# Performance work log

Hardware: AMD Instinct MI355X
Metric: run time of the kernel (lower is better)

Reference implementation:

```python
import jax, jax.numpy as jnp
import numpy as np

B, P, L1, D = 64, 16, 16, 1024  # images, people/img, object slots/img (slot0=no-object), feat dim
SP = 32   # flattened spatial (Conv_spatial output channels)
PROJ = 512
ACT = 29


def setup_inputs() -> dict:
    key = jax.random.key(0)
    ks = jax.random.split(key, 16)
    rn = lambda k, s, sc=1.0: jax.random.normal(k, s, dtype=jnp.float32) * sc
    w = 0.02  # weight init scale
    return {
        "people": rn(ks[0], (B, P, D)),
        "objects": rn(ks[1], (B, L1, D)),
        "context": rn(ks[2], (B, D)),
        "spatial": rn(ks[3], (B, P * L1, SP)),
        "Wvis_w": rn(ks[4], (3 * D, PROJ), w), "Wvis_b": jnp.zeros((PROJ,), jnp.float32),
        "Wspat_w": rn(ks[5], (SP, PROJ), w), "Wspat_b": jnp.zeros((PROJ,), jnp.float32),
        "Wip_w": rn(ks[6], (PROJ, 1), w), "Wip_b": jnp.zeros((1,), jnp.float32),
        "Wref_w": rn(ks[7], (PROJ, ACT), w), "Wref_b": jnp.zeros((ACT,), jnp.float32),
        "Watt_w": rn(ks[8], (PROJ, ACT), w), "Watt_b": jnp.zeros((ACT,), jnp.float32),
        "Woh_w": rn(ks[9], (D, D), w), "Woh_b": jnp.zeros((D,), jnp.float32),
        "Who_w": rn(ks[10], (D, D), w), "Who_b": jnp.zeros((D,), jnp.float32),
        "Wg_w": rn(ks[11], (2 * D, ACT), w), "Wg_b": jnp.zeros((ACT,), jnp.float32),
    }


def reference(people, objects, context, spatial,
              Wvis_w, Wvis_b, Wspat_w, Wspat_b, Wip_w, Wip_b,
              Wref_w, Wref_b, Watt_w, Watt_b,
              Woh_w, Woh_b, Who_w, Who_b, Wg_w, Wg_b):
    Bn, Pn, Dn = people.shape
    L = objects.shape[1]
    C = Bn * Pn * L

    # --- ROI.pairing: all (person, object-slot) pairs + image context -> [C, 3D]
    pe = jnp.broadcast_to(people[:, :, None, :], (Bn, Pn, L, Dn))
    ob = jnp.broadcast_to(objects[:, None, :, :], (Bn, Pn, L, Dn))
    cx = jnp.broadcast_to(context[:, None, None, :], (Bn, Pn, L, Dn))
    pairs = jnp.concatenate([pe, ob, cx], axis=-1).reshape(C, 3 * Dn)

    # --- attention / visual projection heads
    a_ho = jax.nn.relu(spatial.reshape(C, -1) @ Wspat_w + Wspat_b)   # W_Spat
    f_vis = jax.nn.relu(pairs @ Wvis_w + Wvis_b)                     # W_vis
    f_ref = f_vis * a_ho
    i_ho = f_ref @ Wip_w + Wip_b                                     # [C,1]
    interaction_prob = jax.nn.sigmoid(i_ho)
    p_ref = f_ref @ Wref_w + Wref_b                                  # [C,29]
    p_att = a_ho @ Watt_w + Watt_b                                   # [C,29]

    # --- graph message passing: adjacency = interaction probs, skipping slot 0 (no-object)
    adj = interaction_prob.reshape(Bn, Pn, L)[:, :, 1:]              # [B,P,O]
    oh = jax.nn.relu(objects[:, 1:] @ Woh_w + Woh_b)                 # W_oh on objects
    ho = jax.nn.relu(people @ Who_w + Who_b)                         # W_ho on people
    people_r = people + jnp.einsum('bpo,bod->bpd', adj, oh)
    objects_r = objects[:, 1:] + jnp.einsum('bpo,bpd->bod', adj, ho)
    objects_full = jnp.concatenate([objects[:, :1], objects_r], axis=1)  # re-attach no-object slot

    # --- refined all-pairs concat -> W_graph
    pe_r = jnp.broadcast_to(people_r[:, :, None, :], (Bn, Pn, L, Dn))
    ob_r = jnp.broadcast_to(objects_full[:, None, :, :], (Bn, Pn, L, Dn))
    pairs_g = jnp.concatenate([pe_r, ob_r], axis=-1).reshape(C, 2 * Dn)
    p_graph = pairs_g @ Wg_w + Wg_b                                  # [C,29]

    return (i_ho, p_ref, p_att, p_graph)
```

## Files before the change

### kernel.cpp

```cpp
#include <hip/hip_runtime.h>


typedef unsigned short u16;
typedef short s16x8 __attribute__((ext_vector_type(8)));
typedef float f32x4 __attribute__((ext_vector_type(4)));

__device__ __forceinline__ u16 f2b(float f) {
    union { float f; unsigned int i; } v; v.f = f;
    unsigned int r = (v.i + 0x7fffu + ((v.i >> 16) & 1u)) >> 16;
    return (u16)r;
}
__device__ __forceinline__ float b2f(u16 u) {
    union { float f; unsigned int i; } v; v.i = ((unsigned int)u) << 16; return v.f;
}
__device__ __forceinline__ unsigned int pack2(float x, float y) {
    return (unsigned int)f2b(x) | ((unsigned int)f2b(y) << 16);
}

#define OFF_WSPATT 0u
#define OFF_WREFT  32768u
#define OFF_WATTT  65536u
#define OFF_WGT    98304u
#define OFF_PP     229376u
#define OFF_PO     1277952u
#define OFF_PC     2326528u
#define OFF_ADJ    2392064u
#define OFF_HP     2457600u
#define OFF_HOF    2588672u
#define OFF_YH     2719744u
#define OFF_ZO     2850816u
#define ZERO_OFF   2457600u
#define ZERO_LEN   516096u
#define OFF_WVIST2 2973696u
#define OFF_WHOT2  6119424u
#define OFF_WOHT2  8216576u
#define OFF_PEOB   10313728u
#define OFF_OBJB   12410880u
#define OFF_CTXB   14508032u
#define OFF_SPATB  14639104u

__global__ __launch_bounds__(256) void prep_all(
    const float* __restrict__ people, const float* __restrict__ objects,
    const float* __restrict__ context, const float* __restrict__ spatial,
    const float* __restrict__ Wvis, const float* __restrict__ Who,
    const float* __restrict__ Woh, const float* __restrict__ Wspat,
    const float* __restrict__ Wref, const float* __restrict__ Watt,
    const float* __restrict__ Wg,
    u16* __restrict__ peoB, u16* __restrict__ objB, u16* __restrict__ ctxB,
    u16* __restrict__ spatB, u16* __restrict__ WvisT, u16* __restrict__ WhoT,
    u16* __restrict__ WohT, u16* __restrict__ WspatT, u16* __restrict__ WrefT,
    u16* __restrict__ WattT, u16* __restrict__ WgT)
{
    __shared__ float S[64][65];
    int bid = blockIdx.x, t = threadIdx.x;
    if (bid < 896) {
        const float* src; u16* dst; int N, K, kt, nt;
        int tb = bid;
        if (tb < 256)      { src = Who;  dst = WhoT;  K = 1024; N = 1024; kt = tb >> 4; nt = tb & 15; }
        else if (tb < 512) { tb -= 256; src = Woh;  dst = WohT;  K = 1024; N = 1024; kt = tb >> 4; nt = tb & 15; }
        else               { tb -= 512; src = Wvis; dst = WvisT; K = 3072; N = 512;  kt = tb >> 3; nt = tb & 7; }
        int k0 = kt * 64, n0 = nt * 64;
        int tx = t & 63, ty = t >> 6;
#pragma unroll
        for (int i = 0; i < 16; i++)
            S[ty + 4 * i][tx] = src[(size_t)(k0 + ty + 4 * i) * N + n0 + tx];
        __syncthreads();
#pragma unroll
        for (int i = 0; i < 16; i++)
            dst[(size_t)(n0 + ty + 4 * i) * K + k0 + tx] = f2b(S[tx][ty + 4 * i]);
        return;
    }
    int g = (bid - 896) * 256 + t;
    const int gsz = 512 * 256;
    for (int i = g; i < 524288; i += gsz) {
        float2 v = ((const float2*)people)[i];
        ((unsigned int*)peoB)[i] = pack2(v.x, v.y);
    }
    for (int i = g; i < 524288; i += gsz) {
        float2 v = ((const float2*)objects)[i];
        ((unsigned int*)objB)[i] = pack2(v.x, v.y);
    }
    for (int i = g; i < 32768; i += gsz) {
        float2 v = ((const float2*)context)[i];
        ((unsigned int*)ctxB)[i] = pack2(v.x, v.y);
    }
    for (int i = g; i < 262144; i += gsz) {
        float2 v = ((const float2*)spatial)[i];
        ((unsigned int*)spatB)[i] = pack2(v.x, v.y);
    }
    for (int i = g; i < 512 * 32; i += gsz) {
        int n = i >> 5, k = i & 31;
        WspatT[i] = f2b(Wspat[k * 512 + n]);
    }
    for (int i = g; i < 32 * 512; i += gsz) {
        int n = i >> 9, k = i & 511;
        WrefT[i] = (n < 29) ? f2b(Wref[k * 29 + n]) : (u16)0;
        WattT[i] = (n < 29) ? f2b(Watt[k * 29 + n]) : (u16)0;
    }
    for (int i = g; i < 32 * 2048; i += gsz) {
        int n = i >> 11, k = i & 2047;
        WgT[i] = (n < 29) ? f2b(Wg[k * 29 + n]) : (u16)0;
    }
}

__global__ __launch_bounds__(256) void fused_gemms(
    const u16* __restrict__ peoB, const u16* __restrict__ objB,
    const u16* __restrict__ ctxB, const u16* __restrict__ WvisT,
    const u16* __restrict__ WhoT, const float* __restrict__ Who_b,
    const u16* __restrict__ WohT, const float* __restrict__ Woh_b,
    const u16* __restrict__ WgT,
    u16* __restrict__ Pp, u16* __restrict__ Po, u16* __restrict__ Pc,
    float* __restrict__ Yh, float* __restrict__ Zo,
    float* __restrict__ Hp, float* __restrict__ HoF)
{
    __shared__ u16 T[64][72];
    int bid = blockIdx.x;
    int t = threadIdx.x;
    int lane = t & 63, w = t >> 6;
    int l16 = lane & 15, q = lane >> 4;
    int wy = w >> 1, wx = w & 1;

    if (bid < 264) {
        int bx = bid & 7, ty = bid >> 3;
        const u16* A; u16* outB; int koff, bm;
        if (ty < 16)      { A = peoB; outB = Pp; koff = 0;    bm = ty * 64; }
        else if (ty < 32) { A = objB; outB = Po; koff = 1024; bm = (ty - 16) * 64; }
        else              { A = ctxB; outB = Pc; koff = 2048; bm = 0; }
        int bn = bx * 64;

        const u16* ap0 = A + (size_t)(bm + wy * 32 + l16) * 1024 + q * 8;
        const u16* ap1 = ap0 + (size_t)16 * 1024;
        const u16* bp0 = WvisT + (size_t)(bn + wx * 32 + l16) * 3072 + koff + q * 8;
        const u16* bp1 = bp0 + (size_t)16 * 3072;

        f32x4 acc00 = {0,0,0,0}, acc01 = {0,0,0,0}, acc10 = {0,0,0,0}, acc11 = {0,0,0,0};
        s16x8 ca0 = *(const s16x8*)ap0,        ca1 = *(const s16x8*)ap1;
        s16x8 cb0 = *(const s16x8*)bp0,        cb1 = *(const s16x8*)bp1;
        s16x8 na0 = *(const s16x8*)(ap0 + 32), na1 = *(const s16x8*)(ap1 + 32);
        s16x8 nb0 = *(const s16x8*)(bp0 + 32), nb1 = *(const s16x8*)(bp1 + 32);
        ap0 += 64; ap1 += 64; bp0 += 64; bp1 += 64;
        for (int it = 0; it < 30; it++) {
            s16x8 ta0 = *(const s16x8*)ap0, ta1 = *(const s16x8*)ap1;
            s16x8 tb0 = *(const s16x8*)bp0, tb1 = *(const s16x8*)bp1;
            ap0 += 32; ap1 += 32; bp0 += 32; bp1 += 32;
            acc00 = __builtin_amdgcn_mfma_f32_16x16x32_bf16(ca0, cb0, acc00, 0, 0, 0);
            acc01 = __builtin_amdgcn_mfma_f32_16x16x32_bf16(ca0, cb1, acc01, 0, 0, 0);
            acc10 = __builtin_amdgcn_mfma_f32_16x16x32_bf16(ca1, cb0, acc10, 0, 0, 0);
            acc11 = __builtin_amdgcn_mfma_f32_16x16x32_bf16(ca1, cb1, acc11, 0, 0, 0);
            ca0 = na0; ca1 = na1; cb0 = nb0; cb1 = nb1;
            na0 = ta0; na1 = ta1; nb0 = tb0; nb1 = tb1;
        }
        acc00 = __builtin_amdgcn_mfma_f32_16x16x32_bf16(ca0, cb0, acc00, 0, 0, 0);
        acc01 = __builtin_amdgcn_mfma_f32_16x16x32_bf16(ca0, cb1, acc01, 0, 0, 0);
        acc10 = __builtin_amdgcn_mfma_f32_16x16x32_bf16(ca1, cb0, acc10, 0, 0, 0);
        acc11 = __builtin_amdgcn_mfma_f32_16x16x32_bf16(ca1, cb1, acc11, 0, 0, 0);
        acc00 = __builtin_amdgcn_mfma_f32_16x16x32_bf16(na0, nb0, acc00, 0, 0, 0);
        acc01 = __builtin_amdgcn_mfma_f32_16x16x32_bf16(na0, nb1, acc01, 0, 0, 0);
        acc10 = __builtin_amdgcn_mfma_f32_16x16x32_bf16(na1, nb0, acc10, 0, 0, 0);
        acc11 = __builtin_amdgcn_mfma_f32_16x16x32_bf16(na1, nb1, acc11, 0, 0, 0);

        f32x4 accs[2][2] = {{acc00, acc01}, {acc10, acc11}};
#pragma unroll
        for (int ii = 0; ii < 2; ii++)
#pragma unroll
            for (int jj = 0; jj < 2; jj++) {
                int col = bn + wx * 32 + jj * 16 + l16;
#pragma unroll
                for (int r = 0; r < 4; r++) {
                    int row = bm + wy * 32 + ii * 16 + q * 4 + r;
                    outB[(size_t)row * 512 + col] = f2b(accs[ii][jj][r]);
                }
            }
    } else if (bid < 760) {
        int r3 = bid - 264;
        int z, rt, nbt;
        if (r3 < 256) { z = 0; rt = r3 >> 4; nbt = r3 & 15; }
        else          { z = 1; r3 -= 256; rt = r3 >> 4; nbt = r3 & 15; }
        const u16* A    = z ? objB : peoB;
        const u16* W1T  = z ? WohT : WhoT;
        const float* bb = z ? Woh_b : Who_b;
        const u16* Wg2  = z ? WgT : WgT + 1024;
        float* U        = z ? Zo : Yh;
        int m0 = rt * 64, nb = nbt * 64;

        int r0 = m0 + wy * 32 + l16;
        int r1 = r0 + 16;
        if (z) { r0 = (r0 / 15) * 16 + (r0 % 15) + 1;
                 r1 = (r1 / 15) * 16 + (r1 % 15) + 1; }
        const u16* ap0 = A + (size_t)r0 * 1024 + q * 8;
        const u16* ap1 = A + (size_t)r1 * 1024 + q * 8;
        const u16* bp0 = W1T + (size_t)(nb + wx * 32 + l16) * 1024 + q * 8;
        const u16* bp1 = bp0 + (size_t)16 * 1024;

        f32x4 acc00 = {0,0,0,0}, acc01 = {0,0,0,0}, acc10 = {0,0,0,0}, acc11 = {0,0,0,0};
        s16x8 ca0 = *(const s16x8*)ap0,        ca1 = *(const s16x8*)ap1;
        s16x8 cb0 = *(const s16x8*)bp0,        cb1 = *(const s16x8*)bp1;
        s16x8 na0 = *(const s16x8*)(ap0 + 32), na1 = *(const s16x8*)(ap1 + 32);
        s16x8 nb0 = *(const s16x8*)(bp0 + 32), nb1 = *(const s16x8*)(bp1 + 32);
        ap0 += 64; ap1 += 64; bp0 += 64; bp1 += 64;
        for (int it = 0; it < 30; it++) {
            s16x8 ta0 = *(const s16x8*)ap0, ta1 = *(const s16x8*)ap1;
            s16x8 tb0 = *(const s16x8*)bp0, tb1 = *(const s16x8*)bp1;
            ap0 += 32; ap1 += 32; bp0 += 32; bp1 += 32;
            acc00 = __builtin_amdgcn_mfma_f32_16x16x32_bf16(ca0, cb0, acc00, 0, 0, 0);
            acc01 = __builtin_amdgcn_mfma_f32_16x16x32_bf16(ca0, cb1, acc01, 0, 0, 0);
            acc10 = __builtin_amdgcn_mfma_f32_16x16x32_bf16(ca1, cb0, acc10, 0, 0, 0);
            acc11 = __builtin_amdgcn_mfma_f32_16x16x32_bf16(ca1, cb1, acc11, 0, 0, 0);
            ca0 = na0; ca1 = na1; cb0 = nb0; cb1 = nb1;
            na0 = ta0; na1 = ta1; nb0 = tb0; nb1 = tb1;
        }
        acc00 = __builtin_amdgcn_mfma_f32_16x16x32_bf16(ca0, cb0, acc00, 0, 0, 0);
        acc01 = __builtin_amdgcn_mfma_f32_16x16x32_bf16(ca0, cb1, acc01, 0, 0, 0);
        acc10 = __builtin_amdgcn_mfma_f32_16x16x32_bf16(ca1, cb0, acc10, 0, 0, 0);
        acc11 = __builtin_amdgcn_mfma_f32_16x16x32_bf16(ca1, cb1, acc11, 0, 0, 0);
        acc00 = __builtin_amdgcn_mfma_f32_16x16x32_bf16(na0, nb0, acc00, 0, 0, 0);
        acc01 = __builtin_amdgcn_mfma_f32_16x16x32_bf16(na0, nb1, acc01, 0, 0, 0);
        acc10 = __builtin_amdgcn_mfma_f32_16x16x32_bf16(na1, nb0, acc10, 0, 0, 0);
        acc11 = __builtin_amdgcn_mfma_f32_16x16x32_bf16(na1, nb1, acc11, 0, 0, 0);

        f32x4 accs[2][2] = {{acc00, acc01}, {acc10, acc11}};
#pragma unroll
        for (int ii = 0; ii < 2; ii++)
#pragma unroll
            for (int jj = 0; jj < 2; jj++) {
                int col = wx * 32 + jj * 16 + l16;
                float bv = bb[nb + col];
#pragma unroll
                for (int rr = 0; rr < 4; rr++) {
                    float v = accs[ii][jj][rr] + bv;
                    T[wy * 32 + ii * 16 + q * 4 + rr][col] = f2b(fmaxf(v, 0.f));
                }
            }
        __syncthreads();

        f32x4 s20 = {0,0,0,0}, s21 = {0,0,0,0};
#pragma unroll
        for (int kk = 0; kk < 64; kk += 32) {
            s16x8 a2 = *(const s16x8*)(&T[w * 16 + l16][kk + q * 8]);
            s16x8 b20 = *(const s16x8*)(Wg2 + (size_t)l16 * 2048 + nb + kk + q * 8);
            s16x8 b21 = *(const s16x8*)(Wg2 + (size_t)(16 + l16) * 2048 + nb + kk + q * 8);
            s20 = __builtin_amdgcn_mfma_f32_16x16x32_bf16(a2, b20, s20, 0, 0, 0);
            s21 = __builtin_amdgcn_mfma_f32_16x16x32_bf16(a2, b21, s21, 0, 0, 0);
        }
#pragma unroll
        for (int rr = 0; rr < 4; rr++) {
            int row = m0 + w * 16 + q * 4 + rr;
            atomicAdd(&U[(size_t)row * 32 + l16], s20[rr]);
            atomicAdd(&U[(size_t)row * 32 + 16 + l16], s21[rr]);
        }
    } else {
        int r3 = bid - 760;
        int bx = r3 & 7, by = (r3 >> 3) & 7, z = r3 >> 6;
        const u16* A  = z ? objB : peoB;
        const u16* BT = z ? WgT + 1024 : WgT;
        float* outF   = z ? HoF : Hp;
        int bm = bx * 128 + w * 32;
        int kb = by * 128;
        const u16* ap0 = A + (size_t)(bm + l16) * 1024 + kb + q * 8;
        const u16* ap1 = A + (size_t)(bm + 16 + l16) * 1024 + kb + q * 8;
        const u16* bp0 = BT + (size_t)l16 * 2048 + kb + q * 8;
        const u16* bp1 = BT + (size_t)(16 + l16) * 2048 + kb + q * 8;
        f32x4 acc00 = {0,0,0,0}, acc01 = {0,0,0,0}, acc10 = {0,0,0,0}, acc11 = {0,0,0,0};
        s16x8 ca0 = *(const s16x8*)ap0,        ca1 = *(const s16x8*)ap1;
        s16x8 cb0 = *(const s16x8*)bp0,        cb1 = *(const s16x8*)bp1;
        s16x8 na0 = *(const s16x8*)(ap0 + 32), na1 = *(const s16x8*)(ap1 + 32);
        s16x8 nb0 = *(const s16x8*)(bp0 + 32), nb1 = *(const s16x8*)(bp1 + 32);
        ap0 += 64; ap1 += 64; bp0 += 64; bp1 += 64;
#pragma unroll
        for (int it = 0; it < 2; it++) {
            s16x8 ta0 = *(const s16x8*)ap0, ta1 = *(const s16x8*)ap1;
            s16x8 tb0 = *(const s16x8*)bp0, tb1 = *(const s16x8*)bp1;
            ap0 += 32; ap1 += 32; bp0 += 32; bp1 += 32;
            acc00 = __builtin_amdgcn_mfma_f32_16x16x32_bf16(ca0, cb0, acc00, 0, 0, 0);
            acc01 = __builtin_amdgcn_mfma_f32_16x16x32_bf16(ca0, cb1, acc01, 0, 0, 0);
            acc10 = __builtin_amdgcn_mfma_f32_16x16x32_bf16(ca1, cb0, acc10, 0, 0, 0);
            acc11 = __builtin_amdgcn_mfma_f32_16x16x32_bf16(ca1, cb1, acc11, 0, 0, 0);
            ca0 = na0; ca1 = na1; cb0 = nb0; cb1 = nb1;
            na0 = ta0; na1 = ta1; nb0 = tb0; nb1 = tb1;
        }
        acc00 = __builtin_amdgcn_mfma_f32_16x16x32_bf16(ca0, cb0, acc00, 0, 0, 0);
        acc01 = __builtin_amdgcn_mfma_f32_16x16x32_bf16(ca0, cb1, acc01, 0, 0, 0);
        acc10 = __builtin_amdgcn_mfma_f32_16x16x32_bf16(ca1, cb0, acc10, 0, 0, 0);
        acc11 = __builtin_amdgcn_mfma_f32_16x16x32_bf16(ca1, cb1, acc11, 0, 0, 0);
        acc00 = __builtin_amdgcn_mfma_f32_16x16x32_bf16(na0, nb0, acc00, 0, 0, 0);
        acc01 = __builtin_amdgcn_mfma_f32_16x16x32_bf16(na0, nb1, acc01, 0, 0, 0);
        acc10 = __builtin_amdgcn_mfma_f32_16x16x32_bf16(na1, nb0, acc10, 0, 0, 0);
        acc11 = __builtin_amdgcn_mfma_f32_16x16x32_bf16(na1, nb1, acc11, 0, 0, 0);
        f32x4 accs[2][2] = {{acc00, acc01}, {acc10, acc11}};
#pragma unroll
        for (int ii = 0; ii < 2; ii++)
#pragma unroll
            for (int jj = 0; jj < 2; jj++)
#pragma unroll
                for (int r = 0; r < 4; r++)
                    atomicAdd(&outF[(size_t)(bm + ii * 16 + q * 4 + r) * 32 + jj * 16 + l16],
                              accs[ii][jj][r]);
    }
}

__global__ __launch_bounds__(256) void mega(
    const u16* __restrict__ spatB, const u16* __restrict__ WspatT,
    const float* __restrict__ bspat,
    const u16* __restrict__ Pp, const u16* __restrict__ Po,
    const u16* __restrict__ Pc, const float* __restrict__ bvis,
    const u16* __restrict__ WrefT, const float* __restrict__ bref,
    const u16* __restrict__ WattT, const float* __restrict__ batt,
    const float* __restrict__ wip, const float* __restrict__ bip,
    float* __restrict__ outI, float* __restrict__ outRef,
    float* __restrict__ outAtt, float* __restrict__ adjw)
{
    __shared__ u16 tile[32][512];
    __shared__ float part[32][8];
    __shared__ float wipS[512];
    int t = threadIdx.x;
    int c0 = blockIdx.x * 32;
    int lane = t & 63, w = t >> 6;
    int l16 = lane & 15, q = lane >> 4;

    {
        float2 u = *(const float2*)(wip + t * 2);
        wipS[t * 2]     = u.x;
        wipS[t * 2 + 1] = u.y;
    }

    {
        s16x8 a0 = *(const s16x8*)(spatB + (size_t)(c0 + l16) * 32 + q * 8);
        s16x8 a1 = *(const s16x8*)(spatB + (size_t)(c0 + 16 + l16) * 32 + q * 8);
        const u16* wb = WspatT + (size_t)(w * 128 + l16) * 32 + q * 8;
        s16x8 cb = *(const s16x8*)wb;
        s16x8 nb_ = *(const s16x8*)(wb + 16 * 32);
        wb += 32 * 32;
#pragma unroll
        for (int nt = 0; nt < 8; nt++) {
            s16x8 tb;
            if (nt < 6) { tb = *(const s16x8*)wb; wb += 16 * 32; }
            int n = w * 128 + nt * 16;
            f32x4 acc0 = {0,0,0,0}, acc1 = {0,0,0,0};
            acc0 = __builtin_amdgcn_mfma_f32_16x16x32_bf16(a0, cb, acc0, 0, 0, 0);
            acc1 = __builtin_amdgcn_mfma_f32_16x16x32_bf16(a1, cb, acc1, 0, 0, 0);
            cb = nb_; nb_ = tb;
            float bias = bspat[n + l16];
#pragma unroll
            for (int r = 0; r < 4; r++) {
                tile[q * 4 + r][n + l16]      = f2b(fmaxf(acc0[r] + bias, 0.f));
                tile[16 + q * 4 + r][n + l16] = f2b(fmaxf(acc1[r] + bias, 0.f));
            }
        }
    }
    __syncthreads();

    {
        int rt = w >> 1, ct = w & 1;
        const u16* bp = WattT + (size_t)(ct * 16 + l16) * 512 + q * 8;
        f32x4 acc = {0,0,0,0};
        s16x8 cb = *(const s16x8*)bp;
        s16x8 nb_ = *(const s16x8*)(bp + 32);
        bp += 64;
        for (int i = 0; i < 14; i++) {
            s16x8 tb = *(const s16x8*)bp; bp += 32;
            s16x8 a = *(const s16x8*)(&tile[rt * 16 + l16][i * 32 + q * 8]);
            acc = __builtin_amdgcn_mfma_f32_16x16x32_bf16(a, cb, acc, 0, 0, 0);
            cb = nb_; nb_ = tb;
        }
        {
            s16x8 a = *(const s16x8*)(&tile[rt * 16 + l16][14 * 32 + q * 8]);
            acc = __builtin_amdgcn_mfma_f32_16x16x32_bf16(a, cb, acc, 0, 0, 0);
            a = *(const s16x8*)(&tile[rt * 16 + l16][15 * 32 + q * 8]);
            acc = __builtin_amdgcn_mfma_f32_16x16x32_bf16(a, nb_, acc, 0, 0, 0);
        }
        int col = ct * 16 + l16;
        if (col < 29) {
            float bias = batt[col];
#pragma unroll
            for (int r = 0; r < 4; r++) {
                int row = c0 + rt * 16 + q * 4 + r;
                outAtt[(size_t)row * 29 + col] = acc[r] + bias;
            }
        }
    }
    __syncthreads();

    {
        int row = t >> 3, g = t & 7;
        int c = c0 + row;
        int rp = c >> 4, bimg = c >> 8;
        int ro = bimg * 16 + (c & 15);
        const u16* ppr = Pp + (size_t)rp * 512;
        const u16* por = Po + (size_t)ro * 512;
        const u16* pcr = Pc + (size_t)bimg * 512;
        float ps = 0.f;
#pragma unroll 4
        for (int j = 0; j < 64; j += 2) {
            int col = g * 64 + j;
            unsigned int upp = *(const unsigned int*)(ppr + col);
            unsigned int upo = *(const unsigned int*)(por + col);
            unsigned int upc = *(const unsigned int*)(pcr + col);
            float2 bv = *(const float2*)(bvis + col);
            unsigned int uah = *(const unsigned int*)(&tile[row][col]);
            float fv0 = fmaxf(b2f((u16)(upp & 0xffff)) + b2f((u16)(upo & 0xffff))
                            + b2f((u16)(upc & 0xffff)) + bv.x, 0.f);
            float fv1 = fmaxf(b2f((u16)(upp >> 16)) + b2f((u16)(upo >> 16))
                            + b2f((u16)(upc >> 16)) + bv.y, 0.f);
            float fr0 = fv0 * b2f((u16)(uah & 0xffff));
            float fr1 = fv1 * b2f((u16)(uah >> 16));
            *(unsigned int*)(&tile[row][col]) = pack2(fr0, fr1);
            ps += fr0 * wipS[col] + fr1 * wipS[col + 1];
        }
        part[row][g] = ps;
    }
    __syncthreads();

    if (t < 32) {
        float s = part[t][0] + part[t][1] + part[t][2] + part[t][3]
                + part[t][4] + part[t][5] + part[t][6] + part[t][7] + bip[0];
        outI[c0 + t] = s;
        adjw[c0 + t] = 1.f / (1.f + expf(-s));
    }

    {
        int rt = w >> 1, ct = w & 1;
        const u16* bp = WrefT + (size_t)(ct * 16 + l16) * 512 + q * 8;
        f32x4 acc = {0,0,0,0};
        s16x8 cb = *(const s16x8*)bp;
        s16x8 nb_ = *(const s16x8*)(bp + 32);
        bp += 64;
        for (int i = 0; i < 14; i++) {
            s16x8 tb = *(const s16x8*)bp; bp += 32;
            s16x8 a = *(const s16x8*)(&tile[rt * 16 + l16][i * 32 + q * 8]);
            acc = __builtin_amdgcn_mfma_f32_16x16x32_bf16(a, cb, acc, 0, 0, 0);
            cb = nb_; nb_ = tb;
        }
        {
            s16x8 a = *(const s16x8*)(&tile[rt * 16 + l16][14 * 32 + q * 8]);
            acc = __builtin_amdgcn_mfma_f32_16x16x32_bf16(a, cb, acc, 0, 0, 0);
            a = *(const s16x8*)(&tile[rt * 16 + l16][15 * 32 + q * 8]);
            acc = __builtin_amdgcn_mfma_f32_16x16x32_bf16(a, nb_, acc, 0, 0, 0);
        }
        int col = ct * 16 + l16;
        if (col < 29) {
            float bias = bref[col];
#pragma unroll
            for (int r = 0; r < 4; r++) {
                int row = c0 + rt * 16 + q * 4 + r;
                outRef[(size_t)row * 29 + col] = acc[r] + bias;
            }
        }
    }
}

__global__ __launch_bounds__(256) void pgraph2(
    const float* __restrict__ adjw, const float* __restrict__ Hp,
    const float* __restrict__ HoF, const float* __restrict__ Yh,
    const float* __restrict__ Zo, const float* __restrict__ bg,
    float* __restrict__ outG)
{
    int b = blockIdx.x, t = threadIdx.x;
    __shared__ float adjS[16][16];
    __shared__ float YhS[16][32];
    __shared__ float ZoS[15][32];
    __shared__ float PA[16][32];
    __shared__ float OA[16][32];
    adjS[t >> 4][t & 15] = adjw[b * 256 + t];
    for (int i = t; i < 512; i += 256)
        YhS[i >> 5][i & 31] = Yh[(size_t)(b * 16 + (i >> 5)) * 32 + (i & 31)];
    for (int i = t; i < 480; i += 256)
        ZoS[i >> 5][i & 31] = Zo[(size_t)(b * 15 + (i >> 5)) * 32 + (i & 31)];
    __syncthreads();
    for (int i = t; i < 512; i += 256) {
        int p = i >> 5, j = i & 31;
        float s = 0.f;
#pragma unroll
        for (int o = 0; o < 15; o++) s += adjS[p][o + 1] * ZoS[o][j];
        PA[p][j] = s;
        float s2 = 0.f;
#pragma unroll
        for (int pp = 0; pp < 16; pp++) s2 += adjS[pp][p] * YhS[pp][j];
        OA[p][j] = s2;
    }
    __syncthreads();
    int p = t >> 4, l = t & 15;
    const float* hp = Hp + (size_t)(b * 16 + p) * 32;
    const float* ho = HoF + (size_t)(b * 16 + l) * 32;
    size_t c = (size_t)b * 256 + t;
    for (int j = 0; j < 29; j++) {
        float v = hp[j] + ho[j] + bg[j] + PA[p][j];
        if (l >= 1) v += OA[l][j];
        outG[c * 29 + j] = v;
    }
}

extern "C" void kernel_launch(void* const* d_in, const int* in_sizes, int n_in,
                              void* d_out, int out_size, void* d_ws, size_t ws_size,
                              hipStream_t stream)
{
    const float* people  = (const float*)d_in[0];
    const float* objects = (const float*)d_in[1];
    const float* context = (const float*)d_in[2];
    const float* spatial = (const float*)d_in[3];
    const float* Wvis_w  = (const float*)d_in[4];
    const float* Wvis_b  = (const float*)d_in[5];
    const float* Wspat_w = (const float*)d_in[6];
    const float* Wspat_b = (const float*)d_in[7];
    const float* Wip_w   = (const float*)d_in[8];
    const float* Wip_b   = (const float*)d_in[9];
    const float* Wref_w  = (const float*)d_in[10];
    const float* Wref_b  = (const float*)d_in[11];
    const float* Watt_w  = (const float*)d_in[12];
    const float* Watt_b  = (const float*)d_in[13];
    const float* Woh_w   = (const float*)d_in[14];
    const float* Woh_b   = (const float*)d_in[15];
    const float* Who_w   = (const float*)d_in[16];
    const float* Who_b   = (const float*)d_in[17];
    const float* Wg_w    = (const float*)d_in[18];
    const float* Wg_b    = (const float*)d_in[19];

    char* ws = (char*)d_ws;
    u16* WspatT = (u16*)(ws + OFF_WSPATT);
    u16* WrefT  = (u16*)(ws + OFF_WREFT);
    u16* WattT  = (u16*)(ws + OFF_WATTT);
    u16* WgT    = (u16*)(ws + OFF_WGT);
    u16* Ppb    = (u16*)(ws + OFF_PP);
    u16* Pob    = (u16*)(ws + OFF_PO);
    u16* Pcb    = (u16*)(ws + OFF_PC);
    float* adjw = (float*)(ws + OFF_ADJ);
    float* Hp   = (float*)(ws + OFF_HP);
    float* HoF  = (float*)(ws + OFF_HOF);
    float* Yh   = (float*)(ws + OFF_YH);
    float* Zo   = (float*)(ws + OFF_ZO);
    u16* WvisT2 = (u16*)(ws + OFF_WVIST2);
    u16* WhoT2  = (u16*)(ws + OFF_WHOT2);
    u16* WohT2  = (u16*)(ws + OFF_WOHT2);
    u16* peoB   = (u16*)(ws + OFF_PEOB);
    u16* objB   = (u16*)(ws + OFF_OBJB);
    u16* ctxB   = (u16*)(ws + OFF_CTXB);
    u16* spatB  = (u16*)(ws + OFF_SPATB);

    float* outI   = (float*)d_out;
    float* outRef = outI + 16384;
    float* outAtt = outI + 491520;
    float* outG   = outI + 966656;

    hipMemsetAsync(ws + ZERO_OFF, 0, ZERO_LEN, stream);

    prep_all<<<1408, 256, 0, stream>>>(people, objects, context, spatial,
        Wvis_w, Who_w, Woh_w, Wspat_w, Wref_w, Watt_w, Wg_w,
        peoB, objB, ctxB, spatB, WvisT2, WhoT2, WohT2,
        WspatT, WrefT, WattT, WgT);

    fused_gemms<<<888, 256, 0, stream>>>(peoB, objB, ctxB, WvisT2,
        WhoT2, Who_b, WohT2, Woh_b, WgT,
        Ppb, Pob, Pcb, Yh, Zo, Hp, HoF);

    mega<<<512, 256, 0, stream>>>(spatB, WspatT, Wspat_b,
                                  Ppb, Pob, Pcb, Wvis_b,
                                  WrefT, Wref_b, WattT, Watt_b,
                                  Wip_w, Wip_b,
                                  outI, outRef, outAtt, adjw);

    pgraph2<<<64, 256, 0, stream>>>(adjw, Hp, HoF, Yh, Zo, Wg_b, outG);
}
```

Measured before the change: 188.1 us.

## Deepen MFMA load prefetch, vectorize bf16 conversion, fold memset into prep, remap blocks

The GEMM inner loops now prefetch four K-steps of operands ahead instead of two, so more global loads are in flight to hide latency. The fp32-to-bf16 conversion loops use float4 loads, and the workspace zeroing moves from a separate memset into the prep kernel, removing one launch. Block indices in fused_gemms and mega are permuted across an 8-way stride, which appears aimed at spreading work over XCDs. The deeper prefetch costs more VGPRs and may lower occupancy.

Result: slower. 199.6 us (+6.1%).

```diff
diff --git a/kernel.cpp b/kernel.cpp
--- a/kernel.cpp
+++ b/kernel.cpp
@@ -49,7 +49,7 @@
     u16* __restrict__ peoB, u16* __restrict__ objB, u16* __restrict__ ctxB,
     u16* __restrict__ spatB, u16* __restrict__ WvisT, u16* __restrict__ WhoT,
     u16* __restrict__ WohT, u16* __restrict__ WspatT, u16* __restrict__ WrefT,
-    u16* __restrict__ WattT, u16* __restrict__ WgT)
+    u16* __restrict__ WattT, u16* __restrict__ WgT, float* __restrict__ zeroWS)
 {
     __shared__ float S[64][65];
     int bid = blockIdx.x, t = threadIdx.x;
@@ -72,21 +72,25 @@
     }
     int g = (bid - 896) * 256 + t;
     const int gsz = 512 * 256;
-    for (int i = g; i < 524288; i += gsz) {
-        float2 v = ((const float2*)people)[i];
-        ((unsigned int*)peoB)[i] = pack2(v.x, v.y);
-    }
-    for (int i = g; i < 524288; i += gsz) {
-        float2 v = ((const float2*)objects)[i];
-        ((unsigned int*)objB)[i] = pack2(v.x, v.y);
-    }
-    for (int i = g; i < 32768; i += gsz) {
-        float2 v = ((const float2*)context)[i];
-        ((unsigned int*)ctxB)[i] = pack2(v.x, v.y);
-    }
     for (int i = g; i < 262144; i += gsz) {
-        float2 v = ((const float2*)spatial)[i];
-        ((unsigned int*)spatB)[i] = pack2(v.x, v.y);
+        float4 v = ((const float4*)people)[i];
+        ((uint2*)peoB)[i] = make_uint2(pack2(v.x, v.y), pack2(v.z, v.w));
+    }
+    for (int i = g; i < 262144; i += gsz) {
+        float4 v = ((const float4*)objects)[i];
+        ((uint2*)objB)[i] = make_uint2(pack2(v.x, v.y), pack2(v.z, v.w));
+    }
+    for (int i = g; i < 16384; i += gsz) {
+        float4 v = ((const float4*)context)[i];
+        ((uint2*)ctxB)[i] = make_uint2(pack2(v.x, v.y), pack2(v.z, v.w));
+    }
+    for (int i = g; i < 131072; i += gsz) {
+        float4 v = ((const float4*)spatial)[i];
+        ((uint2*)spatB)[i] = make_uint2(pack2(v.x, v.y), pack2(v.z, v.w));
+    }
+    for (int i = g; i < 32256; i += gsz) {
+        f32x4 z = {0.f, 0.f, 0.f, 0.f};
+        ((f32x4*)zeroWS)[i] = z;
     }
     for (int i = g; i < 512 * 32; i += gsz) {
         int n = i >> 5, k = i & 31;
@@ -102,6 +106,38 @@
         WgT[i] = (n < 29) ? f2b(Wg[k * 29 + n]) : (u16)0;
     }
 }
+
+#define K1024_D4_LOOP(AP0, AP1, BP0, BP1)                                       \
+    s16x8 bA0[4], bA1[4], bB0[4], bB1[4];                                       \
+    _Pragma("unroll")                                                           \
+    for (int s = 0; s < 4; s++) {                                               \
+        bA0[s] = *(const s16x8*)(AP0 + s * 32);                                 \
+        bA1[s] = *(const s16x8*)(AP1 + s * 32);                                 \
+        bB0[s] = *(const s16x8*)(BP0 + s * 32);                                 \
+        bB1[s] = *(const s16x8*)(BP1 + s * 32);                                 \
+    }                                                                           \
+    AP0 += 128; AP1 += 128; BP0 += 128; BP1 += 128;                             \
+    for (int it = 0; it < 7; it++) {                                            \
+        _Pragma("unroll")                                                       \
+        for (int s = 0; s < 4; s++) {                                           \
+            s16x8 tA0 = *(const s16x8*)AP0; AP0 += 32;                          \
+            s16x8 tA1 = *(const s16x8*)AP1; AP1 += 32;                          \
+            s16x8 tB0 = *(const s16x8*)BP0; BP0 += 32;                          \
+            s16x8 tB1 = *(const s16x8*)BP1; BP1 += 32;                          \
+            acc00 = __builtin_amdgcn_mfma_f32_16x16x32_bf16(bA0[s], bB0[s], acc00, 0, 0, 0); \
+            acc01 = __builtin_amdgcn_mfma_f32_16x16x32_bf16(bA0[s], bB1[s], acc01, 0, 0, 0); \
+            acc10 = __builtin_amdgcn_mfma_f32_16x16x32_bf16(bA1[s], bB0[s], acc10, 0, 0, 0); \
+            acc11 = __builtin_amdgcn_mfma_f32_16x16x32_bf16(bA1[s], bB1[s], acc11, 0, 0, 0); \
+            bA0[s] = tA0; bA1[s] = tA1; bB0[s] = tB0; bB1[s] = tB1;             \
+        }                                                                       \
+    }                                                                           \
+    _Pragma("unroll")                                                           \
+    for (int s = 0; s < 4; s++) {                                               \
+        acc00 = __builtin_amdgcn_mfma_f32_16x16x32_bf16(bA0[s], bB0[s], acc00, 0, 0, 0); \
+        acc01 = __builtin_amdgcn_mfma_f32_16x16x32_bf16(bA0[s], bB1[s], acc01, 0, 0, 0); \
+        acc10 = __builtin_amdgcn_mfma_f32_16x16x32_bf16(bA1[s], bB0[s], acc10, 0, 0, 0); \
+        acc11 = __builtin_amdgcn_mfma_f32_16x16x32_bf16(bA1[s], bB1[s], acc11, 0, 0, 0); \
+    }
 
 __global__ __launch_bounds__(256) void fused_gemms(
     const u16* __restrict__ peoB, const u16* __restrict__ objB,
@@ -114,7 +150,8 @@
     float* __restrict__ Hp, float* __restrict__ HoF)
 {
     __shared__ u16 T[64][72];
-    int bid = blockIdx.x;
+    int b0 = blockIdx.x;
+    int bid = (b0 & 7) * 111 + (b0 >> 3);
     int t = threadIdx.x;
     int lane = t & 63, w = t >> 6;
     int l16 = lane & 15, q = lane >> 4;
@@ -134,30 +171,7 @@
         const u16* bp1 = bp0 + (size_t)16 * 3072;
 
         f32x4 acc00 = {0,0,0,0}, acc01 = {0,0,0,0}, acc10 = {0,0,0,0}, acc11 = {0,0,0,0};
-        s16x8 ca0 = *(const s16x8*)ap0,        ca1 = *(const s16x8*)ap1;
-        s16x8 cb0 = *(const s16x8*)bp0,        cb1 = *(const s16x8*)bp1;
-        s16x8 na0 = *(const s16x8*)(ap0 + 32), na1 = *(const s16x8*)(ap1 + 32);
-        s16x8 nb0 = *(const s16x8*)(bp0 + 32), nb1 = *(const s16x8*)(bp1 + 32);
-        ap0 += 64; ap1 += 64; bp0 += 64; bp1 += 64;
-        for (int it = 0; it < 30; it++) {
-            s16x8 ta0 = *(const s16x8*)ap0, ta1 = *(const s16x8*)ap1;
-            s16x8 tb0 = *(const s16x8*)bp0, tb1 = *(const s16x8*)bp1;
-            ap0 += 32; ap1 += 32; bp0 += 32; bp1 += 32;
-            acc00 = __builtin_amdgcn_mfma_f32_16x16x32_bf16(ca0, cb0, acc00, 0, 0, 0);
-            acc01 = __builtin_amdgcn_mfma_f32_16x16x32_bf16(ca0, cb1, acc01, 0, 0, 0);
-            acc10 = __builtin_amdgcn_mfma_f32_16x16x32_bf16(ca1, cb0, acc10, 0, 0, 0);
-            acc11 = __builtin_amdgcn_mfma_f32_16x16x32_bf16(ca1, cb1, acc11, 0, 0, 0);
-            ca0 = na0; ca1 = na1; cb0 = nb0; cb1 = nb1;
-            na0 = ta0; na1 = ta1; nb0 = tb0; nb1 = tb1;
-        }
-        acc00 = __builtin_amdgcn_mfma_f32_16x16x32_bf16(ca0, cb0, acc00, 0, 0, 0);
-        acc01 = __builtin_amdgcn_mfma_f32_16x16x32_bf16(ca0, cb1, acc01, 0, 0, 0);
-        acc10 = __builtin_amdgcn_mfma_f32_16x16x32_bf16(ca1, cb0, acc10, 0, 0, 0);
-        acc11 = __builtin_amdgcn_mfma_f32_16x16x32_bf16(ca1, cb1, acc11, 0, 0, 0);
-        acc00 = __builtin_amdgcn_mfma_f32_16x16x32_bf16(na0, nb0, acc00, 0, 0, 0);
-        acc01 = __builtin_amdgcn_mfma_f32_16x16x32_bf16(na0, nb1, acc01, 0, 0, 0);
-        acc10 = __builtin_amdgcn_mfma_f32_16x16x32_bf16(na1, nb0, acc10, 0, 0, 0);
-        acc11 = __builtin_amdgcn_mfma_f32_16x16x32_bf16(na1, nb1, acc11, 0, 0, 0);
+        K1024_D4_LOOP(ap0, ap1, bp0, bp1)
 
         f32x4 accs[2][2] = {{acc00, acc01}, {acc10, acc11}};
 #pragma unroll
@@ -193,30 +207,7 @@
         const u16* bp1 = bp0 + (size_t)16 * 1024;
 
         f32x4 acc00 = {0,0,0,0}, acc01 = {0,0,0,0}, acc10 = {0,0,0,0}, acc11 = {0,0,0,0};
-        s16x8 ca0 = *(const s16x8*)ap0,        ca1 = *(const s16x8*)ap1;
-        s16x8 cb0 = *(const s16x8*)bp0,        cb1 = *(const s16x8*)bp1;
-        s16x8 na0 = *(const s16x8*)(ap0 + 32), na1 = *(const s16x8*)(ap1 + 32);
-        s16x8 nb0 = *(const s16x8*)(bp0 + 32), nb1 = *(const s16x8*)(bp1 + 32);
-        ap0 += 64; ap1 += 64; bp0 += 64; bp1 += 64;
-        for (int it = 0; it < 30; it++) {
-            s16x8 ta0 = *(const s16x8*)ap0, ta1 = *(const s16x8*)ap1;
-            s16x8 tb0 = *(const s16x8*)bp0, tb1 = *(const s16x8*)bp1;
-            ap0 += 32; ap1 += 32; bp0 += 32; bp1 += 32;
-            acc00 = __builtin_amdgcn_mfma_f32_16x16x32_bf16(ca0, cb0, acc00, 0, 0, 0);
-            acc01 = __builtin_amdgcn_mfma_f32_16x16x32_bf16(ca0, cb1, acc01, 0, 0, 0);
-            acc10 = __builtin_amdgcn_mfma_f32_16x16x32_bf16(ca1, cb0, acc10, 0, 0, 0);
-            acc11 = __builtin_amdgcn_mfma_f32_16x16x32_bf16(ca1, cb1, acc11, 0, 0, 0);
-            ca0 = na0; ca1 = na1; cb0 = nb0; cb1 = nb1;
-            na0 = ta0; na1 = ta1; nb0 = tb0; nb1 = tb1;
-        }
-        acc00 = __builtin_amdgcn_mfma_f32_16x16x32_bf16(ca0, cb0, acc00, 0, 0, 0);
-        acc01 = __builtin_amdgcn_mfma_f32_16x16x32_bf16(ca0, cb1, acc01, 0, 0, 0);
-        acc10 = __builtin_amdgcn_mfma_f32_16x16x32_bf16(ca1, cb0, acc10, 0, 0, 0);
-        acc11 = __builtin_amdgcn_mfma_f32_16x16x32_bf16(ca1, cb1, acc11, 0, 0, 0);
-        acc00 = __builtin_amdgcn_mfma_f32_16x16x32_bf16(na0, nb0, acc00, 0, 0, 0);
-        acc01 = __builtin_amdgcn_mfma_f32_16x16x32_bf16(na0, nb1, acc01, 0, 0, 0);
-        acc10 = __builtin_amdgcn_mfma_f32_16x16x32_bf16(na1, nb0, acc10, 0, 0, 0);
-        acc11 = __builtin_amdgcn_mfma_f32_16x16x32_bf16(na1, nb1, acc11, 0, 0, 0);
+        K1024_D4_LOOP(ap0, ap1, bp0, bp1)
 
         f32x4 accs[2][2] = {{acc00, acc01}, {acc10, acc11}};
 #pragma unroll
@@ -261,31 +252,21 @@
         const u16* bp0 = BT + (size_t)l16 * 2048 + kb + q * 8;
         const u16* bp1 = BT + (size_t)(16 + l16) * 2048 + kb + q * 8;
         f32x4 acc00 = {0,0,0,0}, acc01 = {0,0,0,0}, acc10 = {0,0,0,0}, acc11 = {0,0,0,0};
-        s16x8 ca0 = *(const s16x8*)ap0,        ca1 = *(const s16x8*)ap1;
-        s16x8 cb0 = *(const s16x8*)bp0,        cb1 = *(const s16x8*)bp1;
-        s16x8 na0 = *(const s16x8*)(ap0 + 32), na1 = *(const s16x8*)(ap1 + 32);
-        s16x8 nb0 = *(const s16x8*)(bp0 + 32), nb1 = *(const s16x8*)(bp1 + 32);
-        ap0 += 64; ap1 += 64; bp0 += 64; bp1 += 64;
-#pragma unroll
-        for (int it = 0; it < 2; it++) {
-            s16x8 ta0 = *(const s16x8*)ap0, ta1 = *(const s16x8*)ap1;
-            s16x8 tb0 = *(const s16x8*)bp0, tb1 = *(const s16x8*)bp1;
-            ap0 += 32; ap1 += 32; bp0 += 32; bp1 += 32;
-            acc00 = __builtin_amdgcn_mfma_f32_16x16x32_bf16(ca0, cb0, acc00, 0, 0, 0);
-            acc01 = __builtin_amdgcn_mfma_f32_16x16x32_bf16(ca0, cb1, acc01, 0, 0, 0);
-            acc10 = __builtin_amdgcn_mfma_f32_16x16x32_bf16(ca1, cb0, acc10, 0, 0, 0);
-            acc11 = __builtin_amdgcn_mfma_f32_16x16x32_bf16(ca1, cb1, acc11, 0, 0, 0);
-            ca0 = na0; ca1 = na1; cb0 = nb0; cb1 = nb1;
-            na0 = ta0; na1 = ta1; nb0 = tb0; nb1 = tb1;
-        }
-        acc00 = __builtin_amdgcn_mfma_f32_16x16x32_bf16(ca0, cb0, acc00, 0, 0, 0);
-        acc01 = __builtin_amdgcn_mfma_f32_16x16x32_bf16(ca0, cb1, acc01, 0, 0, 0);
-        acc10 = __builtin_amdgcn_mfma_f32_16x16x32_bf16(ca1, cb0, acc10, 0, 0, 0);
-        acc11 = __builtin_amdgcn_mfma_f32_16x16x32_bf16(ca1, cb1, acc11, 0, 0, 0);
-        acc00 = __builtin_amdgcn_mfma_f32_16x16x32_bf16(na0, nb0, acc00, 0, 0, 0);
-        acc01 = __builtin_amdgcn_mfma_f32_16x16x32_bf16(na0, nb1, acc01, 0, 0, 0);
-        acc10 = __builtin_amdgcn_mfma_f32_16x16x32_bf16(na1, nb0, acc10, 0, 0, 0);
-        acc11 = __builtin_amdgcn_mfma_f32_16x16x32_bf16(na1, nb1, acc11, 0, 0, 0);
+        s16x8 bA0[4], bA1[4], bB0[4], bB1[4];
+#pragma unroll
+        for (int s = 0; s < 4; s++) {
+            bA0[s] = *(const s16x8*)(ap0 + s * 32);
+            bA1[s] = *(const s16x8*)(ap1 + s * 32);
+            bB0[s] = *(const s16x8*)(bp0 + s * 32);
+            bB1[s] = *(const s16x8*)(bp1 + s * 32);
+        }
+#pragma unroll
+        for (int s = 0; s < 4; s++) {
+            acc00 = __builtin_amdgcn_mfma_f32_16x16x32_bf16(bA0[s], bB0[s], acc00, 0, 0, 0);
+            acc01 = __builtin_amdgcn_mfma_f32_16x16x32_bf16(bA0[s], bB1[s], acc01, 0, 0, 0);
+            acc10 = __builtin_amdgcn_mfma_f32_16x16x32_bf16(bA1[s], bB0[s], acc10, 0, 0, 0);
+            acc11 = __builtin_amdgcn_mfma_f32_16x16x32_bf16(bA1[s], bB1[s], acc11, 0, 0, 0);
+        }
         f32x4 accs[2][2] = {{acc00, acc01}, {acc10, acc11}};
 #pragma unroll
         for (int ii = 0; ii < 2; ii++)
@@ -313,7 +294,9 @@
     __shared__ float part[32][8];
     __shared__ float wipS[512];
     int t = threadIdx.x;
-    int c0 = blockIdx.x * 32;
+    int b0 = blockIdx.x;
+    int bid = (b0 & 7) * 64 + (b0 >> 3);
+    int c0 = bid * 32;
     int lane = t & 63, w = t >> 6;
     int l16 = lane & 15, q = lane >> 4;
 
@@ -353,20 +336,23 @@
         int rt = w >> 1, ct = w & 1;
         const u16* bp = WattT + (size_t)(ct * 16 + l16) * 512 + q * 8;
         f32x4 acc = {0,0,0,0};
-        s16x8 cb = *(const s16x8*)bp;
-        s16x8 nb_ = *(const s16x8*)(bp + 32);
-        bp += 64;
-        for (int i = 0; i < 14; i++) {
-            s16x8 tb = *(const s16x8*)bp; bp += 32;
-            s16x8 a = *(const s16x8*)(&tile[rt * 16 + l16][i * 32 + q * 8]);
-            acc = __builtin_amdgcn_mfma_f32_16x16x32_bf16(a, cb, acc, 0, 0, 0);
-            cb = nb_; nb_ = tb;
-        }
-        {
-            s16x8 a = *(const s16x8*)(&tile[rt * 16 + l16][14 * 32 + q * 8]);
-            acc = __builtin_amdgcn_mfma_f32_16x16x32_bf16(a, cb, acc, 0, 0, 0);
-            a = *(const s16x8*)(&tile[rt * 16 + l16][15 * 32 + q * 8]);
-            acc = __builtin_amdgcn_mfma_f32_16x16x32_bf16(a, nb_, acc, 0, 0, 0);
+        s16x8 bw[4];
+#pragma unroll
+        for (int s = 0; s < 4; s++) bw[s] = *(const s16x8*)(bp + s * 32);
+        bp += 128;
+        for (int it = 0; it < 3; it++) {
+#pragma unroll
+            for (int s = 0; s < 4; s++) {
+                s16x8 tb = *(const s16x8*)bp; bp += 32;
+                s16x8 a = *(const s16x8*)(&tile[rt * 16 + l16][(it * 4 + s) * 32 + q * 8]);
+                acc = __builtin_amdgcn_mfma_f32_16x16x32_bf16(a, bw[s], acc, 0, 0, 0);
+                bw[s] = tb;
+            }
+        }
+#pragma unroll
+        for (int s = 0; s < 4; s++) {
+            s16x8 a = *(const s16x8*)(&tile[rt * 16 + l16][(12 + s) * 32 + q * 8]);
+            acc = __builtin_amdgcn_mfma_f32_16x16x32_bf16(a, bw[s], acc, 0, 0, 0);
         }
         int col = ct * 16 + l16;
         if (col < 29) {
@@ -421,20 +407,23 @@
         int rt = w >> 1, ct = w & 1;
         const u16* bp = WrefT + (size_t)(ct * 16 + l16) * 512 + q * 8;
         f32x4 acc = {0,0,0,0};
-        s16x8 cb = *(const s16x8*)bp;
-        s16x8 nb_ = *(const s16x8*)(bp + 32);
-        bp += 64;
-        for (int i = 0; i < 14; i++) {
-            s16x8 tb = *(const s16x8*)bp; bp += 32;
-            s16x8 a = *(const s16x8*)(&tile[rt * 16 + l16][i * 32 + q * 8]);
-            acc = __builtin_amdgcn_mfma_f32_16x16x32_bf16(a, cb, acc, 0, 0, 0);
-            cb = nb_; nb_ = tb;
-        }
-        {
-            s16x8 a = *(const s16x8*)(&tile[rt * 16 + l16][14 * 32 + q * 8]);
-            acc = __builtin_amdgcn_mfma_f32_16x16x32_bf16(a, cb, acc, 0, 0, 0);
-            a = *(const s16x8*)(&tile[rt * 16 + l16][15 * 32 + q * 8]);
-            acc = __builtin_amdgcn_mfma_f32_16x16x32_bf16(a, nb_, acc, 0, 0, 0);
+        s16x8 bw[4];
+#pragma unroll
+        for (int s = 0; s < 4; s++) bw[s] = *(const s16x8*)(bp + s * 32);
+        bp += 128;
+        for (int it = 0; it < 3; it++) {
+#pragma unroll
+            for (int s = 0; s < 4; s++) {
+                s16x8 tb = *(const s16x8*)bp; bp += 32;
+                s16x8 a = *(const s16x8*)(&tile[rt * 16 + l16][(it * 4 + s) * 32 + q * 8]);
+                acc = __builtin_amdgcn_mfma_f32_16x16x32_bf16(a, bw[s], acc, 0, 0, 0);
+                bw[s] = tb;
+            }
+        }
+#pragma unroll
+        for (int s = 0; s < 4; s++) {
+            s16x8 a = *(const s16x8*)(&tile[rt * 16 + l16][(12 + s) * 32 + q * 8]);
+            acc = __builtin_amdgcn_mfma_f32_16x16x32_bf16(a, bw[s], acc, 0, 0, 0);
         }
         int col = ct * 16 + l16;
         if (col < 29) {
@@ -534,18 +523,17 @@
     u16* objB   = (u16*)(ws + OFF_OBJB);
     u16* ctxB   = (u16*)(ws + OFF_CTXB);
     u16* spatB  = (u16*)(ws + OFF_SPATB);
+    float* zeroWS = (float*)(ws + ZERO_OFF);
 
     float* outI   = (float*)d_out;
     float* outRef = outI + 16384;
     float* outAtt = outI + 491520;
     float* outG   = outI + 966656;
 
-    hipMemsetAsync(ws + ZERO_OFF, 0, ZERO_LEN, stream);
-
     prep_all<<<1408, 256, 0, stream>>>(people, objects, context, spatial,
         Wvis_w, Who_w, Woh_w, Wspat_w, Wref_w, Watt_w, Wg_w,
         peoB, objB, ctxB, spatB, WvisT2, WhoT2, WohT2,
-        WspatT, WrefT, WattT, WgT);
+        WspatT, WrefT, WattT, WgT, zeroWS);
 
     fused_gemms<<<888, 256, 0, stream>>>(peoB, objB, ctxB, WvisT2,
         WhoT2, Who_b, WohT2, Woh_b, WgT,
```
